# Performance work log

Hardware: AMD Instinct MI355X
Metric: run time of the kernel (lower is better)

## Reference

```python
import jax, jax.numpy as jnp
import numpy as np
from jax import lax

B, L, C_IN, H = 2048, 128, 150, 230  # batch, seq_len, 3*word_size, hidden_size

MASK_TABLE = jnp.array([[0., 0., 0.],
                        [1., 0., 0.],
                        [0., 1., 0.],
                        [0., 0., 1.]], dtype=jnp.float32)  # frozen mask embedding


def setup_inputs() -> dict:
    key = jax.random.key(0)
    k1, k2, k3 = jax.random.split(key, 3)
    Xea = jax.random.normal(k1, (B, L, C_IN), dtype=jnp.float32)
    X_mask = jax.random.randint(k2, (B, L), 0, 4)
    # xavier_uniform for Conv1d weight [out, in, kw]
    fan_in, fan_out = C_IN * 3, H * 3
    limit = float(np.sqrt(6.0 / (fan_in + fan_out)))
    W = jax.random.uniform(k3, (H, C_IN, 3), dtype=jnp.float32, minval=-limit, maxval=limit)
    b = jnp.zeros((H,), dtype=jnp.float32)
    return {"Xea": Xea, "X_mask": X_mask, "W": W, "b": b}


def reference(Xea, X_mask, W, b):
    # Xea: [B, L, C_in] -> conv over sequence dim, kernel=3, padding=1
    x = jnp.transpose(Xea, (0, 2, 1))  # [B, C_in, L]
    y = lax.conv_general_dilated(
        x, W, window_strides=(1,), padding=[(1, 1)],
        dimension_numbers=('NCH', 'OIH', 'NCH'))  # [B, H, L]
    y = y + b[None, :, None]
    X = jnp.transpose(y, (0, 2, 1))  # [B, L, H]
    m = MASK_TABLE[X_mask]  # [B, L, 3] one-hot piece indicators (0 row = pad)
    # piecewise max pool: broadcast multiply then max over seq
    pooled = jnp.max(m[:, :, None, :] * X[:, :, :, None], axis=1)  # [B, H, 3]
    return jnp.tanh(pooled.reshape(pooled.shape[0], -1))  # [B, 3*H]
```

## Files before the change

kernel.cpp:

```cpp
#include <hip/hip_runtime.h>
#include <hip/hip_bf16.h>
#include <math.h>


#define B_SZ   2048
#define L_SEQ  128
#define C_INCH 150
#define H_OUT  230
#define RS     152
#define NROW   129
#define NS8    2451

typedef __attribute__((ext_vector_type(8))) short short8;
typedef __attribute__((ext_vector_type(4))) float float4v;

static __device__ __forceinline__ unsigned short f2bf(float f) {
    union { float f; unsigned u; } x{f};
    unsigned r = (x.u + 0x7FFFu + ((x.u >> 16) & 1u)) >> 16;
    return (unsigned short)r;
}

static __device__ __forceinline__ unsigned cvt2(float2 f) {
    __hip_bfloat162 h = __float22bfloat162_rn(f);
    union { __hip_bfloat162 h; unsigned u; } c{h};
    return c.u;
}

static __device__ __forceinline__ float tanh_fast_pos(float v) {
    float e = __expf(2.0f * v);
    return 1.0f - 2.0f / (e + 1.0f);
}

__global__ void pack_w_kernel(const float* __restrict__ W,
                              unsigned short* __restrict__ Wpk) {
    int t = blockIdx.x * 256 + threadIdx.x;
    int kk   = t >> 10;
    int rem  = t & 1023;
    int ht   = rem >> 6;
    int lane = rem & 63;
    int q    = lane >> 4;
    int c15  = lane & 15;
    int k    = kk / 5;
    int kc   = kk - k * 5;
    int h    = ht * 16 + c15;
    int cb   = kc * 32 + q * 8;
    unsigned short v[8];
    #pragma unroll
    for (int e = 0; e < 8; ++e) {
        int c = cb + e;
        float f = (h < H_OUT && c < C_INCH) ? W[h * 450 + c * 3 + k] : 0.0f;
        v[e] = f2bf(f);
    }
    *(short8*)(Wpk + (size_t)t * 8) = *(short8*)v;
}

__global__ void __launch_bounds__(512, 4)
pcnn_mfma(const float* __restrict__ Xea, const int* __restrict__ Xmask,
          const unsigned short* __restrict__ Wpk,
          const float* __restrict__ bias, float* __restrict__ out) {
    __shared__ __align__(16) unsigned short sX[NROW * RS];
    __shared__ __align__(16) float sSel[L_SEQ * 3];

    const int b    = blockIdx.x;
    const int tid  = threadIdx.x;
    const int wv   = tid >> 6;
    const int lane = tid & 63;
    const int q    = lane >> 4;
    const int c15  = lane & 15;
    const int mh   = wv & 1;
    const int nh   = wv >> 1;

    const float* xb = Xea + (size_t)b * (L_SEQ * C_INCH);
    #pragma unroll
    for (int it = 0; it < 5; ++it) {
        const int t = it * 512 + tid;
        if (it < 4 || t < NS8) {
            const int row = t / 19;
            const int j   = t - row * 19;
            float2 f0 = {0.f, 0.f}, f1 = {0.f, 0.f}, f2 = {0.f, 0.f}, f3 = {0.f, 0.f};
            if (row > 0) {
                const float2* src = (const float2*)(xb + (row - 1) * C_INCH + j * 8);
                f0 = src[0];
                f1 = src[1];
                f2 = src[2];
                if (j < 18) f3 = src[3];
            }
            uint4 u;
            u.x = cvt2(f0); u.y = cvt2(f1); u.z = cvt2(f2); u.w = cvt2(f3);
            *(uint4*)(sX + (size_t)t * 8) = u;
        }
    }

    if (tid < L_SEQ) {
        int mv = Xmask[(size_t)b * L_SEQ + tid];
        sSel[tid * 3 + 0] = (mv == 1) ? 0.0f : -1e30f;
        sSel[tid * 3 + 1] = (mv == 2) ? 0.0f : -1e30f;
        sSel[tid * 3 + 2] = (mv == 3) ? 0.0f : -1e30f;
    }

    const unsigned short* wp = Wpk + ((size_t)(nh * 4) * 64 + lane) * 8;
    short8 bc[4], bn[4];
    #pragma unroll
    for (int nj = 0; nj < 4; ++nj)
        bc[nj] = *(const short8*)(wp + nj * 512);

    __syncthreads();

    float4v acc[4][4];
    #pragma unroll
    for (int mi = 0; mi < 4; ++mi)
        #pragma unroll
        for (int nj = 0; nj < 4; ++nj)
            acc[mi][nj] = (float4v){0.f, 0.f, 0.f, 0.f};

    const unsigned short* a0p = sX + (mh * 64 + c15) * RS + q * 8;
    const unsigned short* a3p2 = (mh == 1 && c15 == 15) ? (a0p - 129 * RS) : a0p;

    #pragma unroll
    for (int kk = 0; kk < 15; ++kk) {
        const int k  = kk / 5;
        const int kc = kk - k * 5;
        if (kk < 14) {
            #pragma unroll
            for (int nj = 0; nj < 4; ++nj)
                bn[nj] = *(const short8*)(wp + (kk + 1) * 8192 + nj * 512);
        }
        short8 a[4];
        #pragma unroll
        for (int mi = 0; mi < 4; ++mi) {
            const unsigned short* base = (mi == 3 && k == 2) ? a3p2 : a0p;
            a[mi] = *(const short8*)(base + (mi * 16 + k) * RS + kc * 32);
        }
        #pragma unroll
        for (int mi = 0; mi < 4; ++mi)
            #pragma unroll
            for (int nj = 0; nj < 4; ++nj)
                acc[mi][nj] = __builtin_amdgcn_mfma_f32_16x16x32_bf16(
                    a[mi], bc[nj], acc[mi][nj], 0, 0, 0);
        #pragma unroll
        for (int nj = 0; nj < 4; ++nj)
            bc[nj] = bn[nj];
    }

    float pz[4][3];
    #pragma unroll
    for (int nj = 0; nj < 4; ++nj)
        #pragma unroll
        for (int p = 0; p < 3; ++p) pz[nj][p] = -1e30f;

    #pragma unroll
    for (int mi = 0; mi < 4; ++mi) {
        const int l0 = mh * 64 + mi * 16 + q * 4;
        const float4v* sp = (const float4v*)(sSel + l0 * 3);
        const float4v s0 = sp[0], s1 = sp[1], s2 = sp[2];
        const float sl[12] = {s0.x, s0.y, s0.z, s0.w, s1.x, s1.y,
                              s1.z, s1.w, s2.x, s2.y, s2.z, s2.w};
        #pragma unroll
        for (int nj = 0; nj < 4; ++nj)
            #pragma unroll
            for (int r = 0; r < 4; ++r) {
                const float y = acc[mi][nj][r];
                pz[nj][0] = fmaxf(pz[nj][0], y + sl[r * 3 + 0]);
                pz[nj][1] = fmaxf(pz[nj][1], y + sl[r * 3 + 1]);
                pz[nj][2] = fmaxf(pz[nj][2], y + sl[r * 3 + 2]);
            }
    }

    __syncthreads();
    float* sP = (float*)sX;

    #pragma unroll
    for (int nj = 0; nj < 4; ++nj) {
        float p0 = pz[nj][0], p1 = pz[nj][1], p2 = pz[nj][2];
        p0 = fmaxf(p0, __shfl_xor(p0, 16, 64));
        p1 = fmaxf(p1, __shfl_xor(p1, 16, 64));
        p2 = fmaxf(p2, __shfl_xor(p2, 16, 64));
        p0 = fmaxf(p0, __shfl_xor(p0, 32, 64));
        p1 = fmaxf(p1, __shfl_xor(p1, 32, 64));
        p2 = fmaxf(p2, __shfl_xor(p2, 32, 64));
        if (q == 0) {
            const int hl = nh * 64 + nj * 16 + c15;
            float* d = sP + (mh * 256 + hl) * 3;
            d[0] = p0; d[1] = p1; d[2] = p2;
        }
    }
    __syncthreads();

    for (int t = tid; t < 768; t += 512) {
        const int h = t / 3;
        const int p = t - h * 3;
        if (h < H_OUT) {
            float v = fmaxf(sP[h * 3 + p], sP[(256 + h) * 3 + p]);
            v = fmaxf(0.0f, v + bias[h]);
            out[(size_t)b * (3 * H_OUT) + h * 3 + p] = tanh_fast_pos(v);
        }
    }
}

extern "C" void kernel_launch(void* const* d_in, const int* in_sizes, int n_in,
                              void* d_out, int out_size, void* d_ws, size_t ws_size,
                              hipStream_t stream) {
    const float* Xea   = (const float*)d_in[0];
    const int*   Xmask = (const int*)d_in[1];
    const float* W     = (const float*)d_in[2];
    const float* bias  = (const float*)d_in[3];
    float* out = (float*)d_out;
    unsigned short* Wpk = (unsigned short*)d_ws;

    pack_w_kernel<<<60, 256, 0, stream>>>(W, Wpk);
    pcnn_mfma<<<B_SZ, 512, 0, stream>>>(Xea, Xmask, Wpk, bias, out);
}
```

Baseline: 277.1 us.

## Process four batches per block with channel-chunk software pipelining of input loads

Each block now handles four batch elements and splits the bf16 input tile into five channel-chunk slots in LDS. Global loads for the next chunks, and for the next batch's chunks and mask, are issued while the MFMAs on the current chunk run, so load latency can hide behind compute. The weight pack order changes to put the tap index innermost to match the new loop order. The cost is a barrier per chunk, fewer blocks in the grid (512 instead of 2048), and more LDS per block.

```diff
diff --git a/kernel.cpp b/kernel.cpp
--- a/kernel.cpp
+++ b/kernel.cpp
@@ -7,9 +7,11 @@
 #define L_SEQ  128
 #define C_INCH 150
 #define H_OUT  230
-#define RS     152
-#define NROW   129
-#define NS8    2451
+
+#define IB     4
+#define CS     40
+#define NR     130
+#define SLOT   (NR * CS)
 
 typedef __attribute__((ext_vector_type(8))) short short8;
 typedef __attribute__((ext_vector_type(4))) float float4v;
@@ -40,8 +42,8 @@
     int lane = rem & 63;
     int q    = lane >> 4;
     int c15  = lane & 15;
-    int k    = kk / 5;
-    int kc   = kk - k * 5;
+    int kc   = kk / 3;
+    int k    = kk - kc * 3;
     int h    = ht * 16 + c15;
     int cb   = kc * 32 + q * 8;
     unsigned short v[8];
@@ -58,53 +60,54 @@
 pcnn_mfma(const float* __restrict__ Xea, const int* __restrict__ Xmask,
           const unsigned short* __restrict__ Wpk,
           const float* __restrict__ bias, float* __restrict__ out) {
-    __shared__ __align__(16) unsigned short sX[NROW * RS];
-    __shared__ __align__(16) float sSel[L_SEQ * 3];
-
-    const int b    = blockIdx.x;
+    __shared__ __align__(16) unsigned short sX[5 * SLOT];
+    __shared__ __align__(16) float sSel[2][L_SEQ * 3];
+    __shared__ __align__(16) float sP[512 * 3];
+
     const int tid  = threadIdx.x;
+    const int lane = tid & 63;
     const int wv   = tid >> 6;
-    const int lane = tid & 63;
     const int q    = lane >> 4;
     const int c15  = lane & 15;
     const int mh   = wv & 1;
     const int nh   = wv >> 1;
-
-    const float* xb = Xea + (size_t)b * (L_SEQ * C_INCH);
-    #pragma unroll
-    for (int it = 0; it < 5; ++it) {
-        const int t = it * 512 + tid;
-        if (it < 4 || t < NS8) {
-            const int row = t / 19;
-            const int j   = t - row * 19;
-            float2 f0 = {0.f, 0.f}, f1 = {0.f, 0.f}, f2 = {0.f, 0.f}, f3 = {0.f, 0.f};
-            if (row > 0) {
-                const float2* src = (const float2*)(xb + (row - 1) * C_INCH + j * 8);
-                f0 = src[0];
-                f1 = src[1];
-                f2 = src[2];
-                if (j < 18) f3 = src[3];
-            }
-            uint4 u;
-            u.x = cvt2(f0); u.y = cvt2(f1); u.z = cvt2(f2); u.w = cvt2(f3);
-            *(uint4*)(sX + (size_t)t * 8) = u;
-        }
-    }
-
+    const int b0   = blockIdx.x * IB;
+
+    const int sr = tid >> 2;
+    const int sg = tid & 3;
+
+    const unsigned short* wp = Wpk + ((size_t)(nh * 4) * 64 + lane) * 8;
+
+    if (tid < 50) {
+        const int sl = tid / 10, w = tid - sl * 10;
+        const int row = (w < 5) ? 0 : 129;
+        const int j   = (w < 5) ? w : w - 5;
+        uint4 z{0u, 0u, 0u, 0u};
+        *(uint4*)(sX + sl * SLOT + row * CS + j * 8) = z;
+    }
+
+    {
+        const float* xp = Xea + (size_t)(b0 * L_SEQ + sr) * C_INCH;
+        const float2* p0 = (const float2*)(xp + sg * 8);
+        float2 f0 = p0[0], f1 = p0[1], f2 = p0[2], f3 = p0[3];
+        uint4 u0{cvt2(f0), cvt2(f1), cvt2(f2), cvt2(f3)};
+        *(uint4*)(sX + (sr + 1) * CS + sg * 8) = u0;
+        const float2* p1 = (const float2*)(xp + 32 + sg * 8);
+        f0 = p1[0]; f1 = p1[1]; f2 = p1[2]; f3 = p1[3];
+        uint4 u1{cvt2(f0), cvt2(f1), cvt2(f2), cvt2(f3)};
+        *(uint4*)(sX + SLOT + (sr + 1) * CS + sg * 8) = u1;
+    }
     if (tid < L_SEQ) {
-        int mv = Xmask[(size_t)b * L_SEQ + tid];
-        sSel[tid * 3 + 0] = (mv == 1) ? 0.0f : -1e30f;
-        sSel[tid * 3 + 1] = (mv == 2) ? 0.0f : -1e30f;
-        sSel[tid * 3 + 2] = (mv == 3) ? 0.0f : -1e30f;
-    }
-
-    const unsigned short* wp = Wpk + ((size_t)(nh * 4) * 64 + lane) * 8;
+        const int mv = Xmask[(size_t)b0 * L_SEQ + tid];
+        sSel[0][tid * 3 + 0] = (mv == 1) ? 0.0f : -1e30f;
+        sSel[0][tid * 3 + 1] = (mv == 2) ? 0.0f : -1e30f;
+        sSel[0][tid * 3 + 2] = (mv == 3) ? 0.0f : -1e30f;
+    }
+
     short8 bc[4], bn[4];
     #pragma unroll
     for (int nj = 0; nj < 4; ++nj)
         bc[nj] = *(const short8*)(wp + nj * 512);
-
-    __syncthreads();
 
     float4v acc[4][4];
     #pragma unroll
@@ -113,86 +116,123 @@
         for (int nj = 0; nj < 4; ++nj)
             acc[mi][nj] = (float4v){0.f, 0.f, 0.f, 0.f};
 
-    const unsigned short* a0p = sX + (mh * 64 + c15) * RS + q * 8;
-    const unsigned short* a3p2 = (mh == 1 && c15 == 15) ? (a0p - 129 * RS) : a0p;
-
-    #pragma unroll
-    for (int kk = 0; kk < 15; ++kk) {
-        const int k  = kk / 5;
-        const int kc = kk - k * 5;
-        if (kk < 14) {
+    __syncthreads();
+
+    for (int bl = 0; bl < IB; ++bl) {
+        const int b = b0 + bl;
+        const bool nb = (bl + 1 < IB);
+
+        #pragma unroll
+        for (int kc = 0; kc < 5; ++kc) {
+            const bool stNext = (kc >= 3);
+            const bool doSt   = stNext ? nb : true;
+            const int  skc    = stNext ? (kc - 3) : (kc + 2);
+            float2 f0{0.f,0.f}, f1{0.f,0.f}, f2{0.f,0.f}, f3{0.f,0.f};
+            if (doSt) {
+                const int sb = stNext ? (b + 1) : b;
+                const float2* p = (const float2*)(
+                    Xea + (size_t)(sb * L_SEQ + sr) * C_INCH + skc * 32 + sg * 8);
+                if (skc < 4 || sg < 2) { f0 = p[0]; f1 = p[1]; f2 = p[2]; f3 = p[3]; }
+                else if (sg == 2)      { f0 = p[0]; f1 = p[1]; f2 = p[2]; }
+            }
+            int mv = 0;
+            if (kc == 3 && nb && tid < L_SEQ)
+                mv = Xmask[(size_t)(b + 1) * L_SEQ + tid];
+
+            const unsigned short* ap =
+                sX + kc * SLOT + (mh * 64 + c15) * CS + q * 8;
             #pragma unroll
-            for (int nj = 0; nj < 4; ++nj)
-                bn[nj] = *(const short8*)(wp + (kk + 1) * 8192 + nj * 512);
-        }
-        short8 a[4];
-        #pragma unroll
-        for (int mi = 0; mi < 4; ++mi) {
-            const unsigned short* base = (mi == 3 && k == 2) ? a3p2 : a0p;
-            a[mi] = *(const short8*)(base + (mi * 16 + k) * RS + kc * 32);
-        }
-        #pragma unroll
-        for (int mi = 0; mi < 4; ++mi)
-            #pragma unroll
-            for (int nj = 0; nj < 4; ++nj)
-                acc[mi][nj] = __builtin_amdgcn_mfma_f32_16x16x32_bf16(
-                    a[mi], bc[nj], acc[mi][nj], 0, 0, 0);
-        #pragma unroll
-        for (int nj = 0; nj < 4; ++nj)
-            bc[nj] = bn[nj];
-    }
-
-    float pz[4][3];
-    #pragma unroll
-    for (int nj = 0; nj < 4; ++nj)
-        #pragma unroll
-        for (int p = 0; p < 3; ++p) pz[nj][p] = -1e30f;
-
-    #pragma unroll
-    for (int mi = 0; mi < 4; ++mi) {
-        const int l0 = mh * 64 + mi * 16 + q * 4;
-        const float4v* sp = (const float4v*)(sSel + l0 * 3);
-        const float4v s0 = sp[0], s1 = sp[1], s2 = sp[2];
-        const float sl[12] = {s0.x, s0.y, s0.z, s0.w, s1.x, s1.y,
-                              s1.z, s1.w, s2.x, s2.y, s2.z, s2.w};
-        #pragma unroll
-        for (int nj = 0; nj < 4; ++nj)
-            #pragma unroll
-            for (int r = 0; r < 4; ++r) {
-                const float y = acc[mi][nj][r];
-                pz[nj][0] = fmaxf(pz[nj][0], y + sl[r * 3 + 0]);
-                pz[nj][1] = fmaxf(pz[nj][1], y + sl[r * 3 + 1]);
-                pz[nj][2] = fmaxf(pz[nj][2], y + sl[r * 3 + 2]);
-            }
-    }
-
-    __syncthreads();
-    float* sP = (float*)sX;
-
-    #pragma unroll
-    for (int nj = 0; nj < 4; ++nj) {
-        float p0 = pz[nj][0], p1 = pz[nj][1], p2 = pz[nj][2];
-        p0 = fmaxf(p0, __shfl_xor(p0, 16, 64));
-        p1 = fmaxf(p1, __shfl_xor(p1, 16, 64));
-        p2 = fmaxf(p2, __shfl_xor(p2, 16, 64));
-        p0 = fmaxf(p0, __shfl_xor(p0, 32, 64));
-        p1 = fmaxf(p1, __shfl_xor(p1, 32, 64));
-        p2 = fmaxf(p2, __shfl_xor(p2, 32, 64));
-        if (q == 0) {
-            const int hl = nh * 64 + nj * 16 + c15;
-            float* d = sP + (mh * 256 + hl) * 3;
-            d[0] = p0; d[1] = p1; d[2] = p2;
-        }
-    }
-    __syncthreads();
-
-    for (int t = tid; t < 768; t += 512) {
-        const int h = t / 3;
-        const int p = t - h * 3;
-        if (h < H_OUT) {
-            float v = fmaxf(sP[h * 3 + p], sP[(256 + h) * 3 + p]);
-            v = fmaxf(0.0f, v + bias[h]);
-            out[(size_t)b * (3 * H_OUT) + h * 3 + p] = tanh_fast_pos(v);
+            for (int k = 0; k < 3; ++k) {
+                const int f  = kc * 3 + k;
+                const int fn = (f + 1 < 15) ? (f + 1) : 0;
+                #pragma unroll
+                for (int nj = 0; nj < 4; ++nj)
+                    bn[nj] = *(const short8*)(wp + fn * 8192 + nj * 512);
+                short8 a[4];
+                #pragma unroll
+                for (int mi = 0; mi < 4; ++mi)
+                    a[mi] = *(const short8*)(ap + (mi * 16 + k) * CS);
+                #pragma unroll
+                for (int mi = 0; mi < 4; ++mi)
+                    #pragma unroll
+                    for (int nj = 0; nj < 4; ++nj)
+                        acc[mi][nj] = __builtin_amdgcn_mfma_f32_16x16x32_bf16(
+                            a[mi], bc[nj], acc[mi][nj], 0, 0, 0);
+                #pragma unroll
+                for (int nj = 0; nj < 4; ++nj) bc[nj] = bn[nj];
+            }
+
+            if (kc == 4) {
+                float pz[4][3];
+                #pragma unroll
+                for (int nj = 0; nj < 4; ++nj) {
+                    pz[nj][0] = -1e30f; pz[nj][1] = -1e30f; pz[nj][2] = -1e30f;
+                }
+                const float* selB = sSel[bl & 1];
+                #pragma unroll
+                for (int mi = 0; mi < 4; ++mi) {
+                    const int l0 = mh * 64 + mi * 16 + q * 4;
+                    const float4v* sp_ = (const float4v*)(selB + l0 * 3);
+                    const float4v s0 = sp_[0], s1 = sp_[1], s2 = sp_[2];
+                    const float sl[12] = {s0.x, s0.y, s0.z, s0.w, s1.x, s1.y,
+                                          s1.z, s1.w, s2.x, s2.y, s2.z, s2.w};
+                    #pragma unroll
+                    for (int nj = 0; nj < 4; ++nj)
+                        #pragma unroll
+                        for (int r = 0; r < 4; ++r) {
+                            const float y = acc[mi][nj][r];
+                            pz[nj][0] = fmaxf(pz[nj][0], y + sl[r * 3 + 0]);
+                            pz[nj][1] = fmaxf(pz[nj][1], y + sl[r * 3 + 1]);
+                            pz[nj][2] = fmaxf(pz[nj][2], y + sl[r * 3 + 2]);
+                        }
+                }
+                #pragma unroll
+                for (int mi = 0; mi < 4; ++mi)
+                    #pragma unroll
+                    for (int nj = 0; nj < 4; ++nj)
+                        acc[mi][nj] = (float4v){0.f, 0.f, 0.f, 0.f};
+                #pragma unroll
+                for (int nj = 0; nj < 4; ++nj) {
+                    float p0 = pz[nj][0], p1 = pz[nj][1], p2 = pz[nj][2];
+                    p0 = fmaxf(p0, __shfl_xor(p0, 16, 64));
+                    p1 = fmaxf(p1, __shfl_xor(p1, 16, 64));
+                    p2 = fmaxf(p2, __shfl_xor(p2, 16, 64));
+                    p0 = fmaxf(p0, __shfl_xor(p0, 32, 64));
+                    p1 = fmaxf(p1, __shfl_xor(p1, 32, 64));
+                    p2 = fmaxf(p2, __shfl_xor(p2, 32, 64));
+                    if (q == 0) {
+                        const int hl = nh * 64 + nj * 16 + c15;
+                        float* d = sP + (mh * 256 + hl) * 3;
+                        d[0] = p0; d[1] = p1; d[2] = p2;
+                    }
+                }
+            }
+
+            if (doSt) {
+                uint4 u{cvt2(f0), cvt2(f1), cvt2(f2), cvt2(f3)};
+                *(uint4*)(sX + skc * SLOT + (sr + 1) * CS + sg * 8) = u;
+            }
+            if (kc == 3 && nb && tid < L_SEQ) {
+                float* s_ = sSel[(bl + 1) & 1] + tid * 3;
+                s_[0] = (mv == 1) ? 0.0f : -1e30f;
+                s_[1] = (mv == 2) ? 0.0f : -1e30f;
+                s_[2] = (mv == 3) ? 0.0f : -1e30f;
+            }
+
+            __syncthreads();
+
+            if (kc == 4) {
+                for (int t = tid; t < 768; t += 512) {
+                    const int h = t / 3;
+                    const int p = t - h * 3;
+                    if (h < H_OUT) {
+                        float v = fmaxf(sP[h * 3 + p], sP[(256 + h) * 3 + p]);
+                        v = fmaxf(0.0f, v + bias[h]);
+                        out[(size_t)b * (3 * H_OUT) + h * 3 + p] =
+                            tanh_fast_pos(v);
+                    }
+                }
+            }
         }
     }
 }
@@ -208,5 +248,5 @@
     unsigned short* Wpk = (unsigned short*)d_ws;
 
     pack_w_kernel<<<60, 256, 0, stream>>>(W, Wpk);
-    pcnn_mfma<<<B_SZ, 512, 0, stream>>>(Xea, Xmask, Wpk, bias, out);
-}
+    pcnn_mfma<<<B_SZ / IB, 512, 0, stream>>>(Xea, Xmask, Wpk, bias, out);
+}
```

Result: slower. 489.8 us (+76.7%).

## Stage conv weights into LDS via double-buffered global_load_lds and batch X loads

Applied to the files above, without the earlier changes.

Each K-step's packed weight slab is now copied from global memory straight into a double-buffered LDS region with global_load_lds. Waves read their B fragments from LDS instead of each fetching them from global, with a block barrier after every K-step. The input tile loads are also hoisted into registers for all five chunks before any bf16 conversion, so more global loads are in flight at once. The cost is an extra 32 KB of LDS per block, which lowers how many blocks fit on a CU, plus fourteen extra barriers in the main loop.

```diff
diff --git a/kernel.cpp b/kernel.cpp
--- a/kernel.cpp
+++ b/kernel.cpp
@@ -29,6 +29,12 @@
 static __device__ __forceinline__ float tanh_fast_pos(float v) {
     float e = __expf(2.0f * v);
     return 1.0f - 2.0f / (e + 1.0f);
+}
+
+static __device__ __forceinline__ void gl_lds16(const void* g, void* l) {
+    __builtin_amdgcn_global_load_lds(
+        (const __attribute__((address_space(1))) unsigned int*)g,
+        (__attribute__((address_space(3))) unsigned int*)l, 16, 0, 0);
 }
 
 __global__ void pack_w_kernel(const float* __restrict__ W,
@@ -60,6 +66,7 @@
           const float* __restrict__ bias, float* __restrict__ out) {
     __shared__ __align__(16) unsigned short sX[NROW * RS];
     __shared__ __align__(16) float sSel[L_SEQ * 3];
+    __shared__ __align__(1024) unsigned char sB[2 * 16384];
 
     const int b    = blockIdx.x;
     const int tid  = threadIdx.x;
@@ -70,25 +77,27 @@
     const int mh   = wv & 1;
     const int nh   = wv >> 1;
 
+    const char* wsrc = (const char*)Wpk;
+    const int ub = wv * 2048;
+    const int lo = ub + lane * 16;
+
+    gl_lds16(wsrc + lo,        (char*)sB + ub);
+    gl_lds16(wsrc + lo + 1024, (char*)sB + ub + 1024);
+
     const float* xb = Xea + (size_t)b * (L_SEQ * C_INCH);
+    float2 pl[5][4];
     #pragma unroll
     for (int it = 0; it < 5; ++it) {
-        const int t = it * 512 + tid;
-        if (it < 4 || t < NS8) {
-            const int row = t / 19;
-            const int j   = t - row * 19;
-            float2 f0 = {0.f, 0.f}, f1 = {0.f, 0.f}, f2 = {0.f, 0.f}, f3 = {0.f, 0.f};
-            if (row > 0) {
-                const float2* src = (const float2*)(xb + (row - 1) * C_INCH + j * 8);
-                f0 = src[0];
-                f1 = src[1];
-                f2 = src[2];
-                if (j < 18) f3 = src[3];
-            }
-            uint4 u;
-            u.x = cvt2(f0); u.y = cvt2(f1); u.z = cvt2(f2); u.w = cvt2(f3);
-            *(uint4*)(sX + (size_t)t * 8) = u;
-        }
+        const int t   = it * 512 + tid;
+        const int tc  = (t < NS8) ? t : (NS8 - 1);
+        const int row = tc / 19;
+        const int j   = tc - row * 19;
+        const int rm1 = (row > 0) ? (row - 1) : 0;
+        const float* s = xb + rm1 * C_INCH + j * 8;
+        pl[it][0] = *(const float2*)(s);
+        pl[it][1] = *(const float2*)(s + 2);
+        pl[it][2] = *(const float2*)(s + 4);
+        pl[it][3] = *(const float2*)(s + ((j < 18) ? 6 : 4));
     }
 
     if (tid < L_SEQ) {
@@ -98,11 +107,24 @@
         sSel[tid * 3 + 2] = (mv == 3) ? 0.0f : -1e30f;
     }
 
-    const unsigned short* wp = Wpk + ((size_t)(nh * 4) * 64 + lane) * 8;
-    short8 bc[4], bn[4];
-    #pragma unroll
-    for (int nj = 0; nj < 4; ++nj)
-        bc[nj] = *(const short8*)(wp + nj * 512);
+    #pragma unroll
+    for (int it = 0; it < 5; ++it) {
+        const int t   = it * 512 + tid;
+        const int tc  = (t < NS8) ? t : (NS8 - 1);
+        const int row = tc / 19;
+        const int j   = tc - row * 19;
+        uint4 u;
+        u.x = cvt2(pl[it][0]);
+        u.y = cvt2(pl[it][1]);
+        u.z = cvt2(pl[it][2]);
+        u.w = cvt2(pl[it][3]);
+        const bool z = (row == 0);
+        u.x = z ? 0u : u.x;
+        u.y = z ? 0u : u.y;
+        u.z = z ? 0u : u.z;
+        u.w = (z || j == 18) ? 0u : u.w;
+        if (t < NS8) *(uint4*)(sX + (size_t)t * 8) = u;
+    }
 
     __syncthreads();
 
@@ -116,15 +138,26 @@
     const unsigned short* a0p = sX + (mh * 64 + c15) * RS + q * 8;
     const unsigned short* a3p2 = (mh == 1 && c15 == 15) ? (a0p - 129 * RS) : a0p;
 
+    const int bfo = (nh * 4) * 1024 + lane * 16;
+
     #pragma unroll
     for (int kk = 0; kk < 15; ++kk) {
+        const int buf = kk & 1;
+        if (kk < 14) {
+            const char* src = wsrc + (size_t)(kk + 1) * 16384;
+            char* dst = (char*)sB + (buf ^ 1) * 16384;
+            gl_lds16(src + lo,        dst + ub);
+            gl_lds16(src + lo + 1024, dst + ub + 1024);
+        }
         const int k  = kk / 5;
         const int kc = kk - k * 5;
-        if (kk < 14) {
-            #pragma unroll
-            for (int nj = 0; nj < 4; ++nj)
-                bn[nj] = *(const short8*)(wp + (kk + 1) * 8192 + nj * 512);
-        }
+
+        const char* bbase = (const char*)sB + buf * 16384 + bfo;
+        short8 bfrag[4];
+        #pragma unroll
+        for (int nj = 0; nj < 4; ++nj)
+            bfrag[nj] = *(const short8*)(bbase + nj * 1024);
+
         short8 a[4];
         #pragma unroll
         for (int mi = 0; mi < 4; ++mi) {
@@ -136,10 +169,9 @@
             #pragma unroll
             for (int nj = 0; nj < 4; ++nj)
                 acc[mi][nj] = __builtin_amdgcn_mfma_f32_16x16x32_bf16(
-                    a[mi], bc[nj], acc[mi][nj], 0, 0, 0);
-        #pragma unroll
-        for (int nj = 0; nj < 4; ++nj)
-            bc[nj] = bn[nj];
+                    a[mi], bfrag[nj], acc[mi][nj], 0, 0, 0);
+
+        if (kk < 14) __syncthreads();
     }
 
     float pz[4][3];
```

Result: faster. 267.2 us (-3.6%).
